# Kernel tuning notes

Measured on AMD Instinct MI355X. Metric: run time of the kernel, lower is better.

## Reference

```python
import jax, jax.numpy as jnp
import numpy as np

N = 65536      # number of nodes being updated
EMBED = 1024   # embed_size
G = 256        # g_size (per-head dim)
MLP = 256      # mlp_size
H = 4          # n_head


def setup_inputs() -> dict:
    key = jax.random.key(0)
    ks = jax.random.split(key, 8)
    s_in = 1.0 / np.sqrt(EMBED)
    s_g = 1.0 / np.sqrt(G)
    s_m = 1.0 / np.sqrt(MLP)
    s_hg = 1.0 / np.sqrt(H * G)
    return {
        "q": jax.random.normal(ks[0], (N, EMBED), jnp.float32),
        "rep": jax.random.normal(ks[1], (N, EMBED), jnp.float32),
        "Wq": jax.random.normal(ks[2], (EMBED, H * G), jnp.float32) * s_in,
        "Wk": jax.random.normal(ks[3], (EMBED, H * G), jnp.float32) * s_in,
        "Wv": jax.random.normal(ks[4], (EMBED, H * G), jnp.float32) * s_in,
        "W1": jax.random.normal(ks[5], (H, G, MLP), jnp.float32) * s_g,
        "b1": jnp.zeros((H, MLP), jnp.float32),
        "W2": jax.random.normal(ks[6], (H, MLP, G), jnp.float32) * s_m,
        "b2": jnp.zeros((H, G), jnp.float32),
        "Ws": jax.random.normal(ks[7], (H * G, EMBED), jnp.float32) * s_hg,
    }


def reference(q, rep, Wq, Wk, Wv, W1, b1, W2, b2, Ws):
    # Per-head Q/K/V projections: [N, E] -> [N, H, G]
    n = q.shape[0]
    Qh = (q @ Wq).reshape(n, H, G)
    Kh = (rep @ Wk).reshape(n, H, G)
    Vh = (rep @ Wv).reshape(n, H, G)
    # Elementwise scaled attention gate (Q, K are per-node vectors -> 2D attn)
    gate = jax.nn.sigmoid(Qh * Kh * (1.0 / np.sqrt(G)))
    z = gate * Vh  # [N, H, G]
    # Per-head MLP (num_mlp = 1 block): G -> MLP -> G with ReLU
    h1 = jax.nn.relu(jnp.einsum('nhg,hgm->nhm', z, W1) + b1)
    z2 = jnp.einsum('nhm,hmg->nhg', h1, W2) + b2
    update_gate = z2.reshape(n, H * G)
    # update_attn_scale (no bias) + fused residual: h = Q - K + proj(gate)
    h = q - rep + update_gate @ Ws
    return h
```

## Files before the change

### kernel.cpp

```cpp
#include <hip/hip_runtime.h>
#include <hip/hip_bf16.h>


typedef __attribute__((ext_vector_type(8))) short bf16x8;
typedef __attribute__((ext_vector_type(4))) float f32x4;
typedef __attribute__((ext_vector_type(4))) short short4v;

#define AS1 __attribute__((address_space(1)))
#define AS3 __attribute__((address_space(3)))

static __device__ __forceinline__ short f2b(float x) {
  __hip_bfloat16 h = __float2bfloat16(x);
  return __builtin_bit_cast(short, h);
}
static __device__ __forceinline__ float b2f(short s) {
  unsigned u = ((unsigned)(unsigned short)s) << 16;
  return __builtin_bit_cast(float, u);
}

__global__ void cvt_bf16_2(const float* __restrict__ q, const float* __restrict__ rep,
                           short* __restrict__ qb, short* __restrict__ rb, long n) {
  const float* __restrict__ in = blockIdx.z ? rep : q;
  short* __restrict__ out = blockIdx.z ? rb : qb;
  long i = ((long)blockIdx.x * blockDim.x + threadIdx.x) * 4;
  const long stride = (long)gridDim.x * blockDim.x * 4;
  for (; i < n; i += stride) {
    float4 v = *(const float4*)(in + i);
    short4v o = { f2b(v.x), f2b(v.y), f2b(v.z), f2b(v.w) };
    *(short4v*)(out + i) = o;
  }
}

__global__ void prep_weights(
    const float* __restrict__ Wq, const float* __restrict__ Wk, const float* __restrict__ Wv,
    const float* __restrict__ W1, const float* __restrict__ W2, const float* __restrict__ Ws,
    short* __restrict__ wqt, short* __restrict__ wkt, short* __restrict__ wvt,
    short* __restrict__ w1t, short* __restrict__ w2t, short* __restrict__ wst)
{
  const int job = blockIdx.z;
  const float* src; short* dst; int R, C;
  if (job < 3)       { src = (job==0)?Wq:((job==1)?Wk:Wv); dst = (job==0)?wqt:((job==1)?wkt:wvt); R = 1024; C = 1024; }
  else if (job == 3) { src = Ws; dst = wst; R = 1024; C = 1024; }
  else if (job < 8)  { int h = job-4; src = W1 + h*65536; dst = w1t + h*65536; R = 256; C = 256; }
  else               { int h = job-8; src = W2 + h*65536; dst = w2t + h*65536; R = 256; C = 256; }
  const int c0 = blockIdx.x * 32, r0 = blockIdx.y * 32;
  if (c0 >= C || r0 >= R) return;
  __shared__ float t[32][33];
  for (int i = threadIdx.y; i < 32; i += 8)
    t[i][threadIdx.x] = src[(long)(r0 + i) * C + c0 + threadIdx.x];
  __syncthreads();
  if (job < 4) {
    for (int i = threadIdx.y; i < 32; i += 8) {
      const int c = c0 + i, r = r0 + threadIdx.x;
      const long idx = (long)(c >> 4) * (R / 8) * 128 + (r >> 3) * 128
                     + ((c & 15) << 3) + (r & 7);
      dst[idx] = f2b(t[threadIdx.x][i]);
    }
  } else {
    for (int i = threadIdx.y; i < 32; i += 8)
      dst[(long)(c0 + i) * R + r0 + threadIdx.x] = f2b(t[threadIdx.x][i]);
  }
}

template <int KDIM, bool RESID>
__global__ __launch_bounds__(512, 2) void gemm_bt(
    const short* __restrict__ A, const short* __restrict__ Bp,
    void* __restrict__ outv,
    const short* __restrict__ qres, const short* __restrict__ rres)
{
  __shared__ __align__(16) short lA[4 * 8192];
  const int lane = threadIdx.x & 63, wave = threadIdx.x >> 6;
  const int wm = wave >> 2, wn = wave & 3;
  int bx = blockIdx.x, by = blockIdx.y;
  {
    const int nbx = gridDim.x;
    const int flat = by * nbx + bx;
    const int chunk = (int)(gridDim.x * gridDim.y) >> 3;
    const int fid = (flat & 7) * chunk + (flat >> 3);
    bx = fid % nbx; by = fid / nbx;
  }
  const long bm = (long)by * 256;
  const int  bn = bx * 256;

  const short* Ab = A + bm * 1024;
  constexpr int NS = KDIM / 32;
  const int g0 = lane >> 4;
  const int arow = wm * 128 + (lane & 15);

  const char* aP = (const char*)lA + arow * 64 + (((g0 ^ (arow >> 1)) & 3) << 4);
  const short* bG = Bp + (long)(bn / 16 + wn * 4) * (KDIM / 8) * 128
                      + g0 * 128 + ((lane & 15) << 3);

  const int rw = lane >> 2;
  const int gg = (lane & 3) ^ ((rw >> 1) & 3);
  const short* Asrc = Ab + (wave * 16 + rw) * 1024 + (gg << 3);
  short* lAd = lA + wave * 16 * 32;

  auto stA = [&](int slot, int s) {
    const int sc = s < NS ? s : NS - 1;
    const short* src = Asrc + sc * 32;
    short* d = lAd + slot * 8192;
    __builtin_amdgcn_global_load_lds((const AS1 void*)src,              (AS3 void*)d,        16, 0, 0);
    __builtin_amdgcn_global_load_lds((const AS1 void*)(src + 128*1024), (AS3 void*)(d+4096), 16, 0, 0);
  };
  auto ldB = [&](bf16x8* d, int s) {
    const int sc = s < NS ? s : NS - 1;
    #pragma unroll
    for (int j = 0; j < 4; ++j)
      d[j] = *(const bf16x8*)(bG + (long)j * (KDIM / 8) * 128 + sc * 512);
  };

  bf16x8 b0[4], b1[4];
  ldB(b0, 0);
  stA(0, 0); stA(1, 1); stA(2, 2);
  asm volatile("s_waitcnt vmcnt(4)" ::: "memory");
  __builtin_amdgcn_s_barrier();

  f32x4 acc[8][4] = {};

#define PHASE(SLOT, MH, BC, STMT, DOVM)                                     \
  {                                                                         \
    bf16x8 a[4];                                                            \
    _Pragma("unroll")                                                       \
    for (int i2 = 0; i2 < 4; ++i2)                                          \
      a[i2] = *(const bf16x8*)(aP + (SLOT) * 16384 + (MH) * 4096 + i2 * 1024); \
    STMT;                                                                   \
    if (DOVM) asm volatile("s_waitcnt vmcnt(6)" ::: "memory");              \
    asm volatile("" ::: "memory");                                          \
    __builtin_amdgcn_s_barrier();                                           \
    __builtin_amdgcn_s_setprio(1);                                          \
    _Pragma("unroll")                                                       \
    for (int i2 = 0; i2 < 4; ++i2)                                          \
      _Pragma("unroll")                                                     \
      for (int j = 0; j < 4; ++j)                                           \
        acc[(MH) * 4 + i2][j] = __builtin_amdgcn_mfma_f32_16x16x32_bf16(    \
            a[i2], BC[j], acc[(MH) * 4 + i2][j], 0, 0, 0);                  \
    __builtin_amdgcn_s_setprio(0);                                          \
    asm volatile("" ::: "memory");                                          \
    __builtin_amdgcn_s_barrier();                                           \
  }

  for (int s = 0; s < NS; s += 4) {
    PHASE(0, 0, b0, { ldB(b1, s + 1); stA(3, s + 3); }, false) PHASE(0, 1, b0, {}, true)
    PHASE(1, 0, b1, { ldB(b0, s + 2); stA(0, s + 4); }, false) PHASE(1, 1, b1, {}, true)
    PHASE(2, 0, b0, { ldB(b1, s + 3); stA(1, s + 5); }, false) PHASE(2, 1, b0, {}, true)
    PHASE(3, 0, b1, { ldB(b0, s + 4); stA(2, s + 6); }, false) PHASE(3, 1, b1, {}, true)
  }
#undef PHASE

  #pragma unroll
  for (int i = 0; i < 8; ++i)
    #pragma unroll
    for (int j = 0; j < 4; ++j)
      #pragma unroll
      for (int r = 0; r < 4; ++r) {
        const int rl = wm * 128 + i * 16 + ((lane >> 4) << 2) + r;
        const int cl = wn * 64 + j * 16 + (lane & 15);
        const float v = acc[i][j][r];
        const long gi = (bm + rl) * 1024 + bn + cl;
        if (RESID) {
          ((float*)outv)[gi] = b2f(qres[gi]) - b2f(rres[gi]) + v;
        } else {
          ((short*)outv)[gi] = f2b(v);
        }
      }
}

__global__ __launch_bounds__(512, 2) void gemm_g23(
    const short* __restrict__ rb, const short* __restrict__ wkt,
    const short* __restrict__ wvt, const short* __restrict__ gh,
    short* __restrict__ zb)
{
  __shared__ __align__(16) short lA[4 * 8192];
  const int lane = threadIdx.x & 63, wave = threadIdx.x >> 6;
  const int wm = wave >> 2, wn = wave & 3;
  int bx = blockIdx.x, by = blockIdx.y;
  {
    const int flat = by * 8 + bx;
    const int chunk = (int)(gridDim.x * gridDim.y) >> 3;
    const int fid = (flat & 7) * chunk + (flat >> 3);
    bx = fid & 7; by = fid >> 3;
  }
  const long bm = (long)by * 256;
  const int  bn = bx * 128;

  const short* Ab = rb + bm * 1024;
  constexpr int NS = 32;
  const int g0 = lane >> 4;
  const int arow = wm * 128 + (lane & 15);

  const char* aP = (const char*)lA + arow * 64 + (((g0 ^ (arow >> 1)) & 3) << 4);
  const short* kG = wkt + (long)(bn / 16 + wn * 2) * 16384 + g0 * 128 + ((lane & 15) << 3);
  const short* vG = wvt + (long)(bn / 16 + wn * 2) * 16384 + g0 * 128 + ((lane & 15) << 3);

  const int rw = lane >> 2;
  const int gg = (lane & 3) ^ ((rw >> 1) & 3);
  const short* Asrc = Ab + (wave * 16 + rw) * 1024 + (gg << 3);
  short* lAd = lA + wave * 16 * 32;

  auto stA = [&](int slot, int s) {
    const int sc = s < NS ? s : NS - 1;
    const short* src = Asrc + sc * 32;
    short* d = lAd + slot * 8192;
    __builtin_amdgcn_global_load_lds((const AS1 void*)src,              (AS3 void*)d,        16, 0, 0);
    __builtin_amdgcn_global_load_lds((const AS1 void*)(src + 128*1024), (AS3 void*)(d+4096), 16, 0, 0);
  };
  auto ldKV = [&](bf16x8* dk, bf16x8* dv, int s) {
    const int sc = s < NS ? s : NS - 1;
    #pragma unroll
    for (int j = 0; j < 2; ++j) {
      dk[j] = *(const bf16x8*)(kG + (long)j * 16384 + sc * 512);
      dv[j] = *(const bf16x8*)(vG + (long)j * 16384 + sc * 512);
    }
  };

  bf16x8 bk0[2], bv0[2], bk1[2], bv1[2];
  ldKV(bk0, bv0, 0);
  stA(0, 0); stA(1, 1); stA(2, 2);
  asm volatile("s_waitcnt vmcnt(4)" ::: "memory");
  __builtin_amdgcn_s_barrier();

  f32x4 ack[8][2] = {};
  f32x4 acv[8][2] = {};

#define PHASEG(SLOT, MH, BK, BV, STMT, DOVM)                                \
  {                                                                         \
    bf16x8 a[4];                                                            \
    _Pragma("unroll")                                                       \
    for (int i2 = 0; i2 < 4; ++i2)                                          \
      a[i2] = *(const bf16x8*)(aP + (SLOT) * 16384 + (MH) * 4096 + i2 * 1024); \
    STMT;                                                                   \
    if (DOVM) asm volatile("s_waitcnt vmcnt(6)" ::: "memory");              \
    asm volatile("" ::: "memory");                                          \
    __builtin_amdgcn_s_barrier();                                           \
    __builtin_amdgcn_s_setprio(1);                                          \
    _Pragma("unroll")                                                       \
    for (int i2 = 0; i2 < 4; ++i2)                                          \
      _Pragma("unroll")                                                     \
      for (int j = 0; j < 2; ++j) {                                         \
        ack[(MH) * 4 + i2][j] = __builtin_amdgcn_mfma_f32_16x16x32_bf16(    \
            a[i2], BK[j], ack[(MH) * 4 + i2][j], 0, 0, 0);                  \
        acv[(MH) * 4 + i2][j] = __builtin_amdgcn_mfma_f32_16x16x32_bf16(    \
            a[i2], BV[j], acv[(MH) * 4 + i2][j], 0, 0, 0);                  \
      }                                                                     \
    __builtin_amdgcn_s_setprio(0);                                          \
    asm volatile("" ::: "memory");                                          \
    __builtin_amdgcn_s_barrier();                                           \
  }

  for (int s = 0; s < NS; s += 4) {
    PHASEG(0, 0, bk0, bv0, { ldKV(bk1, bv1, s + 1); stA(3, s + 3); }, false)
    PHASEG(0, 1, bk0, bv0, {}, true)
    PHASEG(1, 0, bk1, bv1, { ldKV(bk0, bv0, s + 2); stA(0, s + 4); }, false)
    PHASEG(1, 1, bk1, bv1, {}, true)
    PHASEG(2, 0, bk0, bv0, { ldKV(bk1, bv1, s + 3); stA(1, s + 5); }, false)
    PHASEG(2, 1, bk0, bv0, {}, true)
    PHASEG(3, 0, bk1, bv1, { ldKV(bk0, bv0, s + 4); stA(2, s + 6); }, false)
    PHASEG(3, 1, bk1, bv1, {}, true)
  }
#undef PHASEG

  #pragma unroll
  for (int i = 0; i < 8; ++i)
    #pragma unroll
    for (int j = 0; j < 2; ++j)
      #pragma unroll
      for (int r = 0; r < 4; ++r) {
        const int rl = wm * 128 + i * 16 + ((lane >> 4) << 2) + r;
        const int cl = wn * 32 + j * 16 + (lane & 15);
        const long gi = (bm + rl) * 1024 + bn + cl;
        const float x = b2f(gh[gi]) * ack[i][j][r] * 0.0625f;
        const float gate = 1.0f / (1.0f + __expf(-x));
        zb[gi] = f2b(gate * acv[i][j][r]);
      }
}

__global__ __launch_bounds__(512) void gemm_mlp(
    const short* __restrict__ zb, const short* __restrict__ w1t,
    const short* __restrict__ w2t, const float* __restrict__ b1,
    const float* __restrict__ b2, short* __restrict__ ug)
{
  __shared__ __align__(16) char smem[163840];
  short* lA = (short*)smem;
  short* lB = (short*)(smem + 65536);
  short* stash = (short*)smem;
  short* w2b = (short*)(smem + 131072);

  const int lane = threadIdx.x & 63, wave = threadIdx.x >> 6;
  const int wm = wave >> 2, wn = wave & 3;
  const long bm = (long)blockIdx.y * 256;
  const int head = blockIdx.z;

  const int g0 = lane >> 4;
  const int arow = wm * 128 + (lane & 15);
  const int bcol = wn * 64 + (lane & 15);
  const int rw = lane >> 2;
  const int gg = (lane & 3) ^ ((rw >> 1) & 3);

  {
    const short* Ab = zb + bm * 1024 + head * 256;
    const short* Bb = w1t + head * 65536;
    const char* aP = (const char*)lA + arow * 64 + (((g0 ^ (arow >> 1)) & 3) << 4);
    const char* bP = (const char*)lB + bcol * 64 + (((g0 ^ (bcol >> 1)) & 3) << 4);
    const short* Asrc = Ab + (wave * 16 + rw) * 1024 + (gg << 3);
    const short* Bsrc = Bb + (wave * 16 + rw) * 256 + (gg << 3);
    short* lAd = lA + wave * 16 * 32;
    short* lBd = lB + wave * 16 * 32;

    auto stA = [&](int slot, int s) {
      const int sc = s < 8 ? s : 7;
      const short* src = Asrc + sc * 32;
      short* d = lAd + slot * 8192;
      __builtin_amdgcn_global_load_lds((const AS1 void*)src,              (AS3 void*)d,        16, 0, 0);
      __builtin_amdgcn_global_load_lds((const AS1 void*)(src + 128*1024), (AS3 void*)(d+4096), 16, 0, 0);
    };
    auto stB = [&](int slot, int s) {
      const int sc = s < 8 ? s : 7;
      const short* src = Bsrc + sc * 32;
      short* d = lBd + slot * 8192;
      __builtin_amdgcn_global_load_lds((const AS1 void*)src,              (AS3 void*)d,        16, 0, 0);
      __builtin_amdgcn_global_load_lds((const AS1 void*)(src + 128*256),  (AS3 void*)(d+4096), 16, 0, 0);
    };

    stA(0, 0); stB(0, 0);
    stA(1, 1); stB(1, 1);
    stA(2, 2); stB(2, 2);
    asm volatile("s_waitcnt vmcnt(8)" ::: "memory");
    __builtin_amdgcn_s_barrier();

    f32x4 acc[8][4] = {};
    bf16x8 b[4];

#define PHASE1(SLOT, MH, LOADB, STAGE_STMT, DOVM)                           \
    {                                                                       \
      if (LOADB) {                                                          \
        _Pragma("unroll")                                                   \
        for (int j = 0; j < 4; ++j)                                         \
          b[j] = *(const bf16x8*)(bP + (SLOT) * 16384 + j * 1024);          \
      }                                                                     \
      bf16x8 a[4];                                                          \
      _Pragma("unroll")                                                     \
      for (int i2 = 0; i2 < 4; ++i2)                                        \
        a[i2] = *(const bf16x8*)(aP + (SLOT) * 16384 + (MH) * 4096 + i2 * 1024); \
      STAGE_STMT;                                                           \
      if (DOVM) asm volatile("s_waitcnt vmcnt(8)" ::: "memory");            \
      asm volatile("" ::: "memory");                                        \
      __builtin_amdgcn_s_barrier();                                         \
      __builtin_amdgcn_s_setprio(1);                                        \
      _Pragma("unroll")                                                     \
      for (int i2 = 0; i2 < 4; ++i2)                                        \
        _Pragma("unroll")                                                   \
        for (int j = 0; j < 4; ++j)                                         \
          acc[(MH) * 4 + i2][j] = __builtin_amdgcn_mfma_f32_16x16x32_bf16(  \
              a[i2], b[j], acc[(MH) * 4 + i2][j], 0, 0, 0);                 \
      __builtin_amdgcn_s_setprio(0);                                        \
      asm volatile("" ::: "memory");                                        \
      __builtin_amdgcn_s_barrier();                                         \
    }

    for (int s = 0; s < 8; s += 4) {
      PHASE1(0, 0, true,  stA(3, s + 3), false) PHASE1(0, 1, false, stB(3, s + 3), true)
      PHASE1(1, 0, true,  stA(0, s + 4), false) PHASE1(1, 1, false, stB(0, s + 4), true)
      PHASE1(2, 0, true,  stA(1, s + 5), false) PHASE1(2, 1, false, stB(1, s + 5), true)
      PHASE1(3, 0, true,  stA(2, s + 6), false) PHASE1(3, 1, false, stB(2, s + 6), true)
    }
#undef PHASE1

    __syncthreads();
    #pragma unroll
    for (int i = 0; i < 8; ++i)
      #pragma unroll
      for (int j = 0; j < 4; ++j)
        #pragma unroll
        for (int r = 0; r < 4; ++r) {
          const int rl = wm * 128 + i * 16 + ((lane >> 4) << 2) + r;
          const int cl = wn * 64 + j * 16 + (lane & 15);
          float v = acc[i][j][r] + b1[head * 256 + cl];
          v = v > 0.0f ? v : 0.0f;
          stash[rl * 256 + ((((cl >> 3) ^ rl) & 31) << 3) + (cl & 7)] = f2b(v);
        }
    __syncthreads();
  }

  {
    const short* Wb = w2t + head * 65536;
    const short* Bsrc2 = Wb + (wave * 16 + rw) * 256 + (gg << 3);
    short* lBd2 = w2b + wave * 16 * 32;
    const char* b2P = (const char*)w2b + bcol * 64 + (((g0 ^ (bcol >> 1)) & 3) << 4);

    auto stW = [&](int slot, int s) {
      const int sc = s < 8 ? s : 7;
      const short* src = Bsrc2 + sc * 32;
      short* d = lBd2 + slot * 8192;
      __builtin_amdgcn_global_load_lds((const AS1 void*)src,             (AS3 void*)d,        16, 0, 0);
      __builtin_amdgcn_global_load_lds((const AS1 void*)(src + 128*256), (AS3 void*)(d+4096), 16, 0, 0);
    };

    stW(0, 0);
    asm volatile("s_waitcnt vmcnt(0)" ::: "memory");
    __builtin_amdgcn_s_barrier();

    f32x4 acc2[8][4] = {};
    bf16x8 br[4];

    for (int s = 0; s < 8; ++s) {
      const int sl = s & 1;
      const int ks = s * 4 + g0;

#define PHASE2(MH, LOADB, STAGE_STMT, DOVM)                                 \
      {                                                                     \
        if (LOADB) {                                                        \
          _Pragma("unroll")                                                 \
          for (int j = 0; j < 4; ++j)                                       \
            br[j] = *(const bf16x8*)(b2P + sl * 16384 + j * 1024);          \
        }                                                                   \
        bf16x8 a[4];                                                        \
        _Pragma("unroll")                                                   \
        for (int i2 = 0; i2 < 4; ++i2) {                                    \
          const int row = arow + (MH) * 64 + i2 * 16;                       \
          a[i2] = *(const bf16x8*)(stash + row * 256 + (((ks ^ row) & 31) << 3)); \
        }                                                                   \
        STAGE_STMT;                                                         \
        if (DOVM) asm volatile("s_waitcnt vmcnt(0)" ::: "memory");          \
        asm volatile("" ::: "memory");                                      \
        __builtin_amdgcn_s_barrier();                                       \
        __builtin_amdgcn_s_setprio(1);                                      \
        _Pragma("unroll")                                                   \
        for (int i2 = 0; i2 < 4; ++i2)                                      \
          _Pragma("unroll")                                                 \
          for (int j = 0; j < 4; ++j)                                       \
            acc2[(MH) * 4 + i2][j] = __builtin_amdgcn_mfma_f32_16x16x32_bf16( \
                a[i2], br[j], acc2[(MH) * 4 + i2][j], 0, 0, 0);             \
        __builtin_amdgcn_s_setprio(0);                                      \
        asm volatile("" ::: "memory");                                      \
        __builtin_amdgcn_s_barrier();                                       \
      }

      PHASE2(0, true,  stW(sl ^ 1, s + 1), false)
      PHASE2(1, false, {}, true)
#undef PHASE2
    }

    #pragma unroll
    for (int i = 0; i < 8; ++i)
      #pragma unroll
      for (int j = 0; j < 4; ++j)
        #pragma unroll
        for (int r = 0; r < 4; ++r) {
          const int rl = wm * 128 + i * 16 + ((lane >> 4) << 2) + r;
          const int cl = wn * 64 + j * 16 + (lane & 15);
          const float v = acc2[i][j][r] + b2[head * 256 + cl];
          ug[(bm + rl) * 1024 + head * 256 + cl] = f2b(v);
        }
  }
}

extern "C" void kernel_launch(void* const* d_in, const int* in_sizes, int n_in,
                              void* d_out, int out_size, void* d_ws, size_t ws_size,
                              hipStream_t stream) {
  const float* q   = (const float*)d_in[0];
  const float* rep = (const float*)d_in[1];
  const float* Wq  = (const float*)d_in[2];
  const float* Wk  = (const float*)d_in[3];
  const float* Wv  = (const float*)d_in[4];
  const float* W1  = (const float*)d_in[5];
  const float* b1  = (const float*)d_in[6];
  const float* W2  = (const float*)d_in[7];
  const float* b2  = (const float*)d_in[8];
  const float* Ws  = (const float*)d_in[9];
  float* out = (float*)d_out;

  const long NE = 67108864L;
  char* ws = (char*)d_ws;
  short* qb  = (short*)(ws);
  short* rb  = (short*)(ws + NE * 2);
  short* gh  = (short*)(ws + NE * 4);
  short* zb  = (short*)(ws + NE * 6);
  short* ugb = gh;
  char*  wp  = ws + NE * 8;
  short* wqt = (short*)(wp);
  short* wkt = (short*)(wp + 2097152);
  short* wvt = (short*)(wp + 4194304);
  short* wst = (short*)(wp + 6291456);
  short* w1t = (short*)(wp + 8388608);
  short* w2t = (short*)(wp + 8912896);

  cvt_bf16_2<<<dim3(2048, 1, 2), 256, 0, stream>>>(q, rep, qb, rb, NE);
  prep_weights<<<dim3(32, 32, 12), dim3(32, 8), 0, stream>>>(
      Wq, Wk, Wv, W1, W2, Ws, wqt, wkt, wvt, w1t, w2t, wst);

  gemm_bt<1024, false><<<dim3(4, 256), 512, 0, stream>>>(
      qb, wqt, gh, nullptr, nullptr);
  gemm_g23<<<dim3(8, 256), 512, 0, stream>>>(rb, wkt, wvt, gh, zb);
  gemm_mlp<<<dim3(1, 256, 4), 512, 0, stream>>>(zb, w1t, w2t, b1, b2, ugb);
  gemm_bt<1024, true><<<dim3(4, 256), 512, 0, stream>>>(
      ugb, wst, out, qb, rb);
}
```

Measured before the change: 1.063 ms.

## Fuse Q projection GEMM into the K/V gated GEMM kernel

Drops the separate Q projection GEMM that wrote a bf16 gh buffer. The K/V kernel now also streams the q tiles into a second LDS buffer and keeps a third accumulator set. The gate is then computed directly from the fp32 Q, K and V accumulators. This removes one kernel launch, the gh write/read round trip through HBM, and the rounding of Q to bf16. In exchange it doubles LDS use, raises register pressure (48 accumulator tiles), and means Q tiles are recomputed per 128-column block rather than shared.

Measured after the change: 3.213 ms. +202.2%, slower.

```diff
diff --git a/kernel.cpp b/kernel.cpp
--- a/kernel.cpp
+++ b/kernel.cpp
@@ -166,12 +166,13 @@
       }
 }
 
-__global__ __launch_bounds__(512, 2) void gemm_g23(
-    const short* __restrict__ rb, const short* __restrict__ wkt,
-    const short* __restrict__ wvt, const short* __restrict__ gh,
-    short* __restrict__ zb)
+__global__ __launch_bounds__(512, 2) void gemm_g123(
+    const short* __restrict__ qb, const short* __restrict__ rb,
+    const short* __restrict__ wqt, const short* __restrict__ wkt,
+    const short* __restrict__ wvt, short* __restrict__ zb)
 {
-  __shared__ __align__(16) short lA[4 * 8192];
+  __shared__ __align__(16) short lAq[4 * 8192];
+  __shared__ __align__(16) short lAr[4 * 8192];
   const int lane = threadIdx.x & 63, wave = threadIdx.x >> 6;
   const int wm = wave >> 2, wn = wave & 3;
   int bx = blockIdx.x, by = blockIdx.y;
@@ -184,64 +185,84 @@
   const long bm = (long)by * 256;
   const int  bn = bx * 128;
 
-  const short* Ab = rb + bm * 1024;
+  const short* Aqb = qb + bm * 1024;
+  const short* Arb = rb + bm * 1024;
   constexpr int NS = 32;
   const int g0 = lane >> 4;
   const int arow = wm * 128 + (lane & 15);
 
-  const char* aP = (const char*)lA + arow * 64 + (((g0 ^ (arow >> 1)) & 3) << 4);
-  const short* kG = wkt + (long)(bn / 16 + wn * 2) * 16384 + g0 * 128 + ((lane & 15) << 3);
-  const short* vG = wvt + (long)(bn / 16 + wn * 2) * 16384 + g0 * 128 + ((lane & 15) << 3);
+  const char* aPq = (const char*)lAq + arow * 64 + (((g0 ^ (arow >> 1)) & 3) << 4);
+  const char* aPr = (const char*)lAr + arow * 64 + (((g0 ^ (arow >> 1)) & 3) << 4);
+  const long cb0 = (long)(bn / 16 + wn * 2) * 16384 + g0 * 128 + ((lane & 15) << 3);
+  const short* qG = wqt + cb0;
+  const short* kG = wkt + cb0;
+  const short* vG = wvt + cb0;
 
   const int rw = lane >> 2;
   const int gg = (lane & 3) ^ ((rw >> 1) & 3);
-  const short* Asrc = Ab + (wave * 16 + rw) * 1024 + (gg << 3);
-  short* lAd = lA + wave * 16 * 32;
+  const short* Aqsrc = Aqb + (wave * 16 + rw) * 1024 + (gg << 3);
+  const short* Arsrc = Arb + (wave * 16 + rw) * 1024 + (gg << 3);
+  short* lAqd = lAq + wave * 16 * 32;
+  short* lArd = lAr + wave * 16 * 32;
 
   auto stA = [&](int slot, int s) {
     const int sc = s < NS ? s : NS - 1;
-    const short* src = Asrc + sc * 32;
-    short* d = lAd + slot * 8192;
-    __builtin_amdgcn_global_load_lds((const AS1 void*)src,              (AS3 void*)d,        16, 0, 0);
-    __builtin_amdgcn_global_load_lds((const AS1 void*)(src + 128*1024), (AS3 void*)(d+4096), 16, 0, 0);
+    const short* sq = Aqsrc + sc * 32;
+    const short* sr = Arsrc + sc * 32;
+    short* dq = lAqd + slot * 8192;
+    short* dr = lArd + slot * 8192;
+    __builtin_amdgcn_global_load_lds((const AS1 void*)sq,              (AS3 void*)dq,        16, 0, 0);
+    __builtin_amdgcn_global_load_lds((const AS1 void*)(sq + 128*1024), (AS3 void*)(dq+4096), 16, 0, 0);
+    __builtin_amdgcn_global_load_lds((const AS1 void*)sr,              (AS3 void*)dr,        16, 0, 0);
+    __builtin_amdgcn_global_load_lds((const AS1 void*)(sr + 128*1024), (AS3 void*)(dr+4096), 16, 0, 0);
   };
-  auto ldKV = [&](bf16x8* dk, bf16x8* dv, int s) {
+  auto ldB = [&](bf16x8* dq, bf16x8* dk, bf16x8* dv, int s) {
     const int sc = s < NS ? s : NS - 1;
     #pragma unroll
     for (int j = 0; j < 2; ++j) {
+      dq[j] = *(const bf16x8*)(qG + (long)j * 16384 + sc * 512);
       dk[j] = *(const bf16x8*)(kG + (long)j * 16384 + sc * 512);
       dv[j] = *(const bf16x8*)(vG + (long)j * 16384 + sc * 512);
     }
   };
 
-  bf16x8 bk0[2], bv0[2], bk1[2], bv1[2];
-  ldKV(bk0, bv0, 0);
+  bf16x8 bq0[2], bk0[2], bv0[2], bq1[2], bk1[2], bv1[2];
+  ldB(bq0, bk0, bv0, 0);
   stA(0, 0); stA(1, 1); stA(2, 2);
-  asm volatile("s_waitcnt vmcnt(4)" ::: "memory");
+  asm volatile("s_waitcnt vmcnt(8)" ::: "memory");
   __builtin_amdgcn_s_barrier();
 
+  f32x4 acq[8][2] = {};
   f32x4 ack[8][2] = {};
   f32x4 acv[8][2] = {};
 
-#define PHASEG(SLOT, MH, BK, BV, STMT, DOVM)                                \
+#define PHASEQ(SLOT, MH, BQ, BK, BV, STMT, DOVM)                            \
   {                                                                         \
-    bf16x8 a[4];                                                            \
+    bf16x8 aq[4], ar[4];                                                    \
     _Pragma("unroll")                                                       \
-    for (int i2 = 0; i2 < 4; ++i2)                                          \
-      a[i2] = *(const bf16x8*)(aP + (SLOT) * 16384 + (MH) * 4096 + i2 * 1024); \
+    for (int i2 = 0; i2 < 4; ++i2) {                                        \
+      aq[i2] = *(const bf16x8*)(aPq + (SLOT) * 16384 + (MH) * 4096 + i2 * 1024); \
+      ar[i2] = *(const bf16x8*)(aPr + (SLOT) * 16384 + (MH) * 4096 + i2 * 1024); \
+    }                                                                       \
     STMT;                                                                   \
-    if (DOVM) asm volatile("s_waitcnt vmcnt(6)" ::: "memory");              \
+    if (DOVM) asm volatile("s_waitcnt vmcnt(14)" ::: "memory");             \
     asm volatile("" ::: "memory");                                          \
     __builtin_amdgcn_s_barrier();                                           \
     __builtin_amdgcn_s_setprio(1);                                          \
     _Pragma("unroll")                                                       \
     for (int i2 = 0; i2 < 4; ++i2)                                          \
       _Pragma("unroll")                                                     \
+      for (int j = 0; j < 2; ++j)                                           \
+        acq[(MH) * 4 + i2][j] = __builtin_amdgcn_mfma_f32_16x16x32_bf16(    \
+            aq[i2], BQ[j], acq[(MH) * 4 + i2][j], 0, 0, 0);                 \
+    _Pragma("unroll")                                                       \
+    for (int i2 = 0; i2 < 4; ++i2)                                          \
+      _Pragma("unroll")                                                     \
       for (int j = 0; j < 2; ++j) {                                         \
         ack[(MH) * 4 + i2][j] = __builtin_amdgcn_mfma_f32_16x16x32_bf16(    \
-            a[i2], BK[j], ack[(MH) * 4 + i2][j], 0, 0, 0);                  \
+            ar[i2], BK[j], ack[(MH) * 4 + i2][j], 0, 0, 0);                 \
         acv[(MH) * 4 + i2][j] = __builtin_amdgcn_mfma_f32_16x16x32_bf16(    \
-            a[i2], BV[j], acv[(MH) * 4 + i2][j], 0, 0, 0);                  \
+            ar[i2], BV[j], acv[(MH) * 4 + i2][j], 0, 0, 0);                 \
       }                                                                     \
     __builtin_amdgcn_s_setprio(0);                                          \
     asm volatile("" ::: "memory");                                          \
@@ -249,16 +270,16 @@
   }
 
   for (int s = 0; s < NS; s += 4) {
-    PHASEG(0, 0, bk0, bv0, { ldKV(bk1, bv1, s + 1); stA(3, s + 3); }, false)
-    PHASEG(0, 1, bk0, bv0, {}, true)
-    PHASEG(1, 0, bk1, bv1, { ldKV(bk0, bv0, s + 2); stA(0, s + 4); }, false)
-    PHASEG(1, 1, bk1, bv1, {}, true)
-    PHASEG(2, 0, bk0, bv0, { ldKV(bk1, bv1, s + 3); stA(1, s + 5); }, false)
-    PHASEG(2, 1, bk0, bv0, {}, true)
-    PHASEG(3, 0, bk1, bv1, { ldKV(bk0, bv0, s + 4); stA(2, s + 6); }, false)
-    PHASEG(3, 1, bk1, bv1, {}, true)
-  }
-#undef PHASEG
+    PHASEQ(0, 0, bq0, bk0, bv0, { ldB(bq1, bk1, bv1, s + 1); stA(3, s + 3); }, false)
+    PHASEQ(0, 1, bq0, bk0, bv0, {}, true)
+    PHASEQ(1, 0, bq1, bk1, bv1, { ldB(bq0, bk0, bv0, s + 2); stA(0, s + 4); }, false)
+    PHASEQ(1, 1, bq1, bk1, bv1, {}, true)
+    PHASEQ(2, 0, bq0, bk0, bv0, { ldB(bq1, bk1, bv1, s + 3); stA(1, s + 5); }, false)
+    PHASEQ(2, 1, bq0, bk0, bv0, {}, true)
+    PHASEQ(3, 0, bq1, bk1, bv1, { ldB(bq0, bk0, bv0, s + 4); stA(2, s + 6); }, false)
+    PHASEQ(3, 1, bq1, bk1, bv1, {}, true)
+  }
+#undef PHASEQ
 
   #pragma unroll
   for (int i = 0; i < 8; ++i)
@@ -269,7 +290,7 @@
         const int rl = wm * 128 + i * 16 + ((lane >> 4) << 2) + r;
         const int cl = wn * 32 + j * 16 + (lane & 15);
         const long gi = (bm + rl) * 1024 + bn + cl;
-        const float x = b2f(gh[gi]) * ack[i][j][r] * 0.0625f;
+        const float x = acq[i][j][r] * ack[i][j][r] * 0.0625f;
         const float gate = 1.0f / (1.0f + __expf(-x));
         zb[gi] = f2b(gate * acv[i][j][r]);
       }
@@ -474,9 +495,8 @@
   char* ws = (char*)d_ws;
   short* qb  = (short*)(ws);
   short* rb  = (short*)(ws + NE * 2);
-  short* gh  = (short*)(ws + NE * 4);
+  short* ugb = (short*)(ws + NE * 4);
   short* zb  = (short*)(ws + NE * 6);
-  short* ugb = gh;
   char*  wp  = ws + NE * 8;
   short* wqt = (short*)(wp);
   short* wkt = (short*)(wp + 2097152);
@@ -489,9 +509,7 @@
   prep_weights<<<dim3(32, 32, 12), dim3(32, 8), 0, stream>>>(
       Wq, Wk, Wv, W1, W2, Ws, wqt, wkt, wvt, w1t, w2t, wst);
 
-  gemm_bt<1024, false><<<dim3(4, 256), 512, 0, stream>>>(
-      qb, wqt, gh, nullptr, nullptr);
-  gemm_g23<<<dim3(8, 256), 512, 0, stream>>>(rb, wkt, wvt, gh, zb);
+  gemm_g123<<<dim3(8, 256), 512, 0, stream>>>(qb, rb, wqt, wkt, wvt, zb);
   gemm_mlp<<<dim3(1, 256, 4), 512, 0, stream>>>(zb, w1t, w2t, b1, b2, ugb);
   gemm_bt<1024, true><<<dim3(4, 256), 512, 0, stream>>>(
       ugb, wst, out, qb, rb);
```
